# Performance work log

Measured on AMD Instinct MI355X. Metric: run time of the kernel, lower is better.

Reference implementation:

```python
import jax, jax.numpy as jnp
import numpy as np

N_NODES = 50000
NEG_SLOPE = 0.01  # F.leaky_relu default


def setup_inputs() -> dict:
    key = jax.random.key(0)
    k1, k2, k3, k4, k5 = jax.random.split(key, 5)
    in_dim, out_dim, n_edges = 256, 64, 800000
    h = jax.random.normal(k1, (N_NODES, in_dim), dtype=jnp.float32)
    edge_src = jax.random.randint(k2, (n_edges,), 0, N_NODES, dtype=jnp.int32)
    edge_dst = jax.random.randint(k3, (n_edges,), 0, N_NODES, dtype=jnp.int32)
    W_fc = jax.random.normal(k4, (in_dim, out_dim), dtype=jnp.float32) / np.sqrt(in_dim)
    a_attn = jax.random.normal(k5, (2 * out_dim,), dtype=jnp.float32) / np.sqrt(2 * out_dim)
    return {"h": h, "edge_src": edge_src, "edge_dst": edge_dst, "W_fc": W_fc, "a_attn": a_attn}


def reference(h, edge_src, edge_dst, W_fc, a_attn):
    # z = fc(h)
    z = h @ W_fc                                   # [N, D]
    D = z.shape[1]
    # cat([z_src, z_dst]) @ a == z_src @ a_l + z_dst @ a_r (no edge concat materialized)
    a_l, a_r = a_attn[:D], a_attn[D:]
    s_l = z @ a_l                                  # [N]
    s_r = z @ a_r                                  # [N]
    e = s_l[edge_src] + s_r[edge_dst]              # [E]
    e = jnp.where(e > 0, e, NEG_SLOPE * e)         # leaky_relu
    # segment softmax over incoming edges of each dst node (DGL mailbox softmax)
    m = jax.ops.segment_max(e, edge_dst, num_segments=N_NODES)   # -inf for isolated nodes
    ex = jnp.exp(e - m[edge_dst])                  # [E]
    den = jax.ops.segment_sum(ex, edge_dst, num_segments=N_NODES)
    alpha = ex / den[edge_dst]                     # [E]
    # weighted neighbor aggregation: h_v = sum_{u->v} alpha * z_u
    msgs = alpha[:, None] * z[edge_src]            # [E, D]
    h_out = jax.ops.segment_sum(msgs, edge_dst, num_segments=N_NODES)  # [N, D]
    return h_out
```

## Files before the change

### kernel.cpp

```cpp
#include <hip/hip_runtime.h>

#define IN_DIM   256
#define OUT_DIM  64
#define NEG_SLOPE 0.01f
#define KPAD (IN_DIM + 8)
#define MAXBUCK 2048
#define CAP     1024
#define EPB     4096

typedef __attribute__((ext_vector_type(8))) short short8;
typedef __attribute__((ext_vector_type(4))) float f32x4;
typedef unsigned short ushort_t;

__device__ inline unsigned f2bf_u(float f) {
    unsigned u = __float_as_uint(f);
    return (u + 0x7FFF + ((u >> 16) & 1)) >> 16;
}
__device__ inline short f2bf(float f) { return (short)f2bf_u(f); }
__device__ inline float bf2f(unsigned u16) { return __uint_as_float(u16 << 16); }

__global__ __launch_bounds__(256)
void prep_kernel(const float* __restrict__ W, short* __restrict__ Wt,
                 int* __restrict__ cnt, int nbuck)
{
    const int g = blockIdx.x * 256 + threadIdx.x;
    for (int i = g; i < nbuck; i += 8 * 256) cnt[i] = 0;
    for (int i = g; i < IN_DIM * OUT_DIM; i += 8 * 256) {
        const int k = i & (IN_DIM - 1);
        const int n = i >> 8;
        Wt[i] = f2bf(W[(size_t)k * OUT_DIM + n]);
    }
}

__global__ __launch_bounds__(256, 4)
void fused_kernel(const float* __restrict__ h, const short* __restrict__ Wt,
                  const float* __restrict__ a_attn,
                  ushort_t* __restrict__ z_bf, float* __restrict__ s_l,
                  float* __restrict__ s_r,
                  const int* __restrict__ esrc, const int* __restrict__ edst,
                  int* __restrict__ cnt, unsigned* __restrict__ perm,
                  int n_nodes, int n_edges, int nbuck, int ms_blocks)
{
    __shared__ union {
        short As[64 * KPAD];
        struct { int hist[MAXBUCK]; int cur[MAXBUCK]; } m;
    } sm;

    const int tid = threadIdx.x;

    if ((int)blockIdx.x < ms_blocks) {
        for (int i = tid; i < nbuck; i += 256) sm.m.hist[i] = 0;
        __syncthreads();
        const int base = blockIdx.x * EPB;
        unsigned pw[EPB / 256];
#pragma unroll
        for (int j = 0; j < EPB / 256; ++j) {
            const int i = base + j * 256 + tid;
            unsigned w = 0xFFFFFFFFu;
            if (i < n_edges) {
                const int d = edst[i];
                w = ((unsigned)d << 16) | (unsigned)esrc[i];
                atomicAdd(&sm.m.hist[d >> 5], 1);
            }
            pw[j] = w;
        }
        __syncthreads();
        for (int i = tid; i < nbuck; i += 256) {
            const int hv = sm.m.hist[i];
            if (hv) sm.m.cur[i] = i * CAP + atomicAdd(&cnt[i], hv);
        }
        __syncthreads();
#pragma unroll
        for (int j = 0; j < EPB / 256; ++j) {
            const unsigned w = pw[j];
            if (w != 0xFFFFFFFFu) {
                const int bk = (int)(w >> 21);
                const int pos = atomicAdd(&sm.m.cur[bk], 1);
                if (pos < (bk + 1) * CAP) perm[pos] = w;
            }
        }
        return;
    }

    const int wave = tid >> 6;
    const int lane = tid & 63;
    const int nbase = ((int)blockIdx.x - ms_blocks) * 64;

    for (int i = tid; i < 64 * (IN_DIM / 4); i += 256) {
        const int m  = i >> 6;
        const int k4 = i & 63;
        int node = nbase + m;
        if (node >= n_nodes) node = n_nodes - 1;
        const float4 h4 = *(const float4*)&h[(size_t)node * IN_DIM + k4 * 4];
        uint2 p;
        p.x = f2bf_u(h4.x) | (f2bf_u(h4.y) << 16);
        p.y = f2bf_u(h4.z) | (f2bf_u(h4.w) << 16);
        *(uint2*)&sm.As[m * KPAD + k4 * 4] = p;
    }
    __syncthreads();

    f32x4 acc[4];
#pragma unroll
    for (int t = 0; t < 4; ++t) acc[t] = (f32x4){0.f, 0.f, 0.f, 0.f};

    const int col0 = lane & 15;
    const int quad = lane >> 4;
    const int mrow = wave * 16 + col0;
    const int kq   = quad * 8;

#pragma unroll
    for (int ks = 0; ks < IN_DIM / 32; ++ks) {
        const int kb = ks * 32 + kq;
        const short8 a = *(const short8*)&sm.As[mrow * KPAD + kb];
#pragma unroll
        for (int t = 0; t < 4; ++t) {
            const short8 b = *(const short8*)&Wt[(t * 16 + col0) * IN_DIM + kb];
            acc[t] = __builtin_amdgcn_mfma_f32_16x16x32_bf16(a, b, acc[t], 0, 0, 0);
        }
    }

    float al[4], ar[4];
#pragma unroll
    for (int t = 0; t < 4; ++t) {
        al[t] = a_attn[t * 16 + col0];
        ar[t] = a_attn[OUT_DIM + t * 16 + col0];
    }
#pragma unroll
    for (int r = 0; r < 4; ++r) {
        const int m = nbase + wave * 16 + quad * 4 + r;
        const bool live = m < n_nodes;
        float sl = 0.f, sr = 0.f;
#pragma unroll
        for (int t = 0; t < 4; ++t) {
            const float v = acc[t][r];
            if (live) z_bf[(size_t)m * OUT_DIM + t * 16 + col0] = (ushort_t)f2bf(v);
            sl += v * al[t];
            sr += v * ar[t];
        }
#pragma unroll
        for (int off = 1; off < 16; off <<= 1) {
            sl += __shfl_xor(sl, off, 16);
            sr += __shfl_xor(sr, off, 16);
        }
        if (live && col0 == 0) { s_l[m] = sl; s_r[m] = sr; }
    }
}

__global__ __launch_bounds__(512)
void gather_kernel(const unsigned* __restrict__ perm, const int* __restrict__ cnt,
                   const float* __restrict__ s_l, const float* __restrict__ s_r,
                   const ushort_t* __restrict__ z_bf, float* __restrict__ out,
                   int n_nodes)
{
    __shared__ unsigned eds[CAP];
    __shared__ ushort_t srcs[CAP];
    __shared__ int hist[32], starts[33], cur[32];

    const int tid = threadIdx.x;
    const int b   = blockIdx.x;
    int nE = cnt[b];
    if (nE > CAP) nE = CAP;

    if (tid < 32) hist[tid] = 0;
    __syncthreads();

    for (int i = tid; i < nE; i += 512) {
        const unsigned p = perm[(size_t)b * CAP + i];
        eds[i] = p;
        atomicAdd(&hist[(p >> 16) & 31], 1);
    }
    __syncthreads();

    if (tid < 32) {
        const int v = hist[tid];
        int inc = v;
#pragma unroll
        for (int off = 1; off < 32; off <<= 1) {
            const int u = __shfl_up(inc, off, 32);
            if (tid >= off) inc += u;
        }
        starts[tid + 1] = inc;
        cur[tid] = inc - v;
        if (tid == 0) starts[0] = 0;
    }
    __syncthreads();

    for (int i = tid; i < nE; i += 512) {
        const unsigned p = eds[i];
        const int pos = atomicAdd(&cur[(p >> 16) & 31], 1);
        srcs[pos] = (ushort_t)(p & 0xFFFFu);
    }
    __syncthreads();

    const int ld = tid >> 4;
    const int c  = tid & 15;
    const int d  = b * 32 + ld;
    if (d >= n_nodes) return;

    int k = starts[ld];
    const int ke = starts[ld + 1];
    const float srd = s_r[d];

    float a0 = 0.f, a1 = 0.f, a2 = 0.f, a3 = 0.f, den = 0.f;

    for (; k + 8 <= ke; k += 8) {
        int   s[8];
        float l[8];
        uint2 q[8];
#pragma unroll
        for (int j = 0; j < 8; ++j) s[j] = srcs[k + j];
#pragma unroll
        for (int j = 0; j < 8; ++j) {
            l[j] = s_l[s[j]];
            q[j] = *(const uint2*)&z_bf[(size_t)s[j] * OUT_DIM + c * 4];
        }
#pragma unroll
        for (int j = 0; j < 8; ++j) {
            float e = l[j] + srd;
            e = e > 0.f ? e : NEG_SLOPE * e;
            const float x = __expf(e);
            den += x;
            a0 += x * bf2f(q[j].x & 0xFFFFu);
            a1 += x * bf2f(q[j].x >> 16);
            a2 += x * bf2f(q[j].y & 0xFFFFu);
            a3 += x * bf2f(q[j].y >> 16);
        }
    }
    for (; k + 4 <= ke; k += 4) {
        int   s[4];
        float l[4];
        uint2 q[4];
#pragma unroll
        for (int j = 0; j < 4; ++j) s[j] = srcs[k + j];
#pragma unroll
        for (int j = 0; j < 4; ++j) {
            l[j] = s_l[s[j]];
            q[j] = *(const uint2*)&z_bf[(size_t)s[j] * OUT_DIM + c * 4];
        }
#pragma unroll
        for (int j = 0; j < 4; ++j) {
            float e = l[j] + srd;
            e = e > 0.f ? e : NEG_SLOPE * e;
            const float x = __expf(e);
            den += x;
            a0 += x * bf2f(q[j].x & 0xFFFFu);
            a1 += x * bf2f(q[j].x >> 16);
            a2 += x * bf2f(q[j].y & 0xFFFFu);
            a3 += x * bf2f(q[j].y >> 16);
        }
    }
    for (; k < ke; ++k) {
        const int s0 = srcs[k];
        float e = s_l[s0] + srd;
        e = e > 0.f ? e : NEG_SLOPE * e;
        const float x = __expf(e);
        const uint2 q0 = *(const uint2*)&z_bf[(size_t)s0 * OUT_DIM + c * 4];
        den += x;
        a0 += x * bf2f(q0.x & 0xFFFFu);
        a1 += x * bf2f(q0.x >> 16);
        a2 += x * bf2f(q0.y & 0xFFFFu);
        a3 += x * bf2f(q0.y >> 16);
    }

    const float inv = den > 0.f ? 1.f / den : 0.f;
    float4 o;
    o.x = a0 * inv; o.y = a1 * inv; o.z = a2 * inv; o.w = a3 * inv;
    *(float4*)&out[(size_t)d * OUT_DIM + c * 4] = o;
}

extern "C" void kernel_launch(void* const* d_in, const int* in_sizes, int n_in,
                              void* d_out, int out_size, void* d_ws, size_t ws_size,
                              hipStream_t stream)
{
    const float* h        = (const float*)d_in[0];
    const int*   edge_src = (const int*)  d_in[1];
    const int*   edge_dst = (const int*)  d_in[2];
    const float* W        = (const float*)d_in[3];
    const float* a_attn   = (const float*)d_in[4];
    float*       out      = (float*)d_out;

    const int n_nodes = in_sizes[0] / IN_DIM;
    const int n_edges = in_sizes[1];
    const int nbuck   = (n_nodes + 31) >> 5;

    char* wsb = (char*)d_ws;
    short*    Wt   = (short*)wsb;
    size_t off = (size_t)IN_DIM * OUT_DIM * sizeof(short);
    ushort_t* z_bf = (ushort_t*)(wsb + off);
    off += (size_t)n_nodes * OUT_DIM * sizeof(ushort_t);
    float*    s_l  = (float*)(wsb + off);  off += (size_t)n_nodes * 4;
    float*    s_r  = (float*)(wsb + off);  off += (size_t)n_nodes * 4;
    int*      cnt  = (int*)(wsb + off);    off += ((size_t)nbuck * 4 + 15) & ~(size_t)15;
    unsigned* perm = (unsigned*)(wsb + off);

    const int ms_blocks   = (n_edges + EPB - 1) / EPB;
    const int gemm_blocks = (n_nodes + 63) / 64;

    prep_kernel<<<8, 256, 0, stream>>>(W, Wt, cnt, nbuck);
    fused_kernel<<<ms_blocks + gemm_blocks, 256, 0, stream>>>(
        h, Wt, a_attn, z_bf, s_l, s_r, edge_src, edge_dst, cnt, perm,
        n_nodes, n_edges, nbuck, ms_blocks);
    gather_kernel<<<nbuck, 512, 0, stream>>>(
        perm, cnt, s_l, s_r, z_bf, out, n_nodes);
}
```

Before: 133.9 us.

## Split each node's edge list across two 8-lane groups with 16-byte loads

The gather kernel now has each destination node's incoming edges handled by two groups of 8 lanes, each covering half the edge range. Each lane loads 8 bf16 features with one 16-byte load instead of 4 with an 8-byte load. The two partial sums and denominators are combined through shared memory after a block barrier and then normalized and written out. This is meant to shorten per-node dependency chains and widen memory transactions. It costs extra shared memory and a sync, and removes the 4-edge unrolled remainder loop.

```diff
diff --git a/kernel.cpp b/kernel.cpp
--- a/kernel.cpp
+++ b/kernel.cpp
@@ -154,6 +154,8 @@
 {
     __shared__ unsigned eds[CAP];
     __shared__ ushort_t srcs[CAP];
+    __shared__ float accH[2][32][OUT_DIM];
+    __shared__ float denH[2][32];
     __shared__ int hist[32], starts[33], cur[32];
 
     const int tid = threadIdx.x;
@@ -192,27 +194,34 @@
     }
     __syncthreads();
 
-    const int ld = tid >> 4;
-    const int c  = tid & 15;
-    const int d  = b * 32 + ld;
-    if (d >= n_nodes) return;
-
-    int k = starts[ld];
-    const int ke = starts[ld + 1];
-    const float srd = s_r[d];
-
-    float a0 = 0.f, a1 = 0.f, a2 = 0.f, a3 = 0.f, den = 0.f;
+    const int grp  = tid >> 3;
+    const int ld   = grp >> 1;
+    const int half = grp & 1;
+    const int c2   = tid & 7;
+    const int d    = b * 32 + ld;
+
+    const int begin = starts[ld];
+    const int end   = starts[ld + 1];
+    const int mid   = begin + ((end - begin + 1) >> 1);
+    int k  = half ? mid : begin;
+    const int ke = half ? end : mid;
+    const float srd = (d < n_nodes) ? s_r[d] : 0.f;
+
+    float a[8];
+#pragma unroll
+    for (int t = 0; t < 8; ++t) a[t] = 0.f;
+    float den = 0.f;
 
     for (; k + 8 <= ke; k += 8) {
         int   s[8];
         float l[8];
-        uint2 q[8];
+        uint4 q[8];
 #pragma unroll
         for (int j = 0; j < 8; ++j) s[j] = srcs[k + j];
 #pragma unroll
         for (int j = 0; j < 8; ++j) {
             l[j] = s_l[s[j]];
-            q[j] = *(const uint2*)&z_bf[(size_t)s[j] * OUT_DIM + c * 4];
+            q[j] = *(const uint4*)&z_bf[(size_t)s[j] * OUT_DIM + c2 * 8];
         }
 #pragma unroll
         for (int j = 0; j < 8; ++j) {
@@ -220,33 +229,14 @@
             e = e > 0.f ? e : NEG_SLOPE * e;
             const float x = __expf(e);
             den += x;
-            a0 += x * bf2f(q[j].x & 0xFFFFu);
-            a1 += x * bf2f(q[j].x >> 16);
-            a2 += x * bf2f(q[j].y & 0xFFFFu);
-            a3 += x * bf2f(q[j].y >> 16);
-        }
-    }
-    for (; k + 4 <= ke; k += 4) {
-        int   s[4];
-        float l[4];
-        uint2 q[4];
-#pragma unroll
-        for (int j = 0; j < 4; ++j) s[j] = srcs[k + j];
-#pragma unroll
-        for (int j = 0; j < 4; ++j) {
-            l[j] = s_l[s[j]];
-            q[j] = *(const uint2*)&z_bf[(size_t)s[j] * OUT_DIM + c * 4];
-        }
-#pragma unroll
-        for (int j = 0; j < 4; ++j) {
-            float e = l[j] + srd;
-            e = e > 0.f ? e : NEG_SLOPE * e;
-            const float x = __expf(e);
-            den += x;
-            a0 += x * bf2f(q[j].x & 0xFFFFu);
-            a1 += x * bf2f(q[j].x >> 16);
-            a2 += x * bf2f(q[j].y & 0xFFFFu);
-            a3 += x * bf2f(q[j].y >> 16);
+            a[0] += x * bf2f(q[j].x & 0xFFFFu);
+            a[1] += x * bf2f(q[j].x >> 16);
+            a[2] += x * bf2f(q[j].y & 0xFFFFu);
+            a[3] += x * bf2f(q[j].y >> 16);
+            a[4] += x * bf2f(q[j].z & 0xFFFFu);
+            a[5] += x * bf2f(q[j].z >> 16);
+            a[6] += x * bf2f(q[j].w & 0xFFFFu);
+            a[7] += x * bf2f(q[j].w >> 16);
         }
     }
     for (; k < ke; ++k) {
@@ -254,18 +244,40 @@
         float e = s_l[s0] + srd;
         e = e > 0.f ? e : NEG_SLOPE * e;
         const float x = __expf(e);
-        const uint2 q0 = *(const uint2*)&z_bf[(size_t)s0 * OUT_DIM + c * 4];
+        const uint4 q0 = *(const uint4*)&z_bf[(size_t)s0 * OUT_DIM + c2 * 8];
         den += x;
-        a0 += x * bf2f(q0.x & 0xFFFFu);
-        a1 += x * bf2f(q0.x >> 16);
-        a2 += x * bf2f(q0.y & 0xFFFFu);
-        a3 += x * bf2f(q0.y >> 16);
-    }
-
-    const float inv = den > 0.f ? 1.f / den : 0.f;
-    float4 o;
-    o.x = a0 * inv; o.y = a1 * inv; o.z = a2 * inv; o.w = a3 * inv;
-    *(float4*)&out[(size_t)d * OUT_DIM + c * 4] = o;
+        a[0] += x * bf2f(q0.x & 0xFFFFu);
+        a[1] += x * bf2f(q0.x >> 16);
+        a[2] += x * bf2f(q0.y & 0xFFFFu);
+        a[3] += x * bf2f(q0.y >> 16);
+        a[4] += x * bf2f(q0.z & 0xFFFFu);
+        a[5] += x * bf2f(q0.z >> 16);
+        a[6] += x * bf2f(q0.w & 0xFFFFu);
+        a[7] += x * bf2f(q0.w >> 16);
+    }
+
+#pragma unroll
+    for (int t = 0; t < 8; ++t) accH[half][ld][c2 * 8 + t] = a[t];
+    if (c2 == 0) denH[half][ld] = den;
+    __syncthreads();
+
+    for (int i = tid; i < 32 * 16; i += 512) {
+        const int l2 = i >> 4;
+        const int cq = i & 15;
+        const int dd = b * 32 + l2;
+        if (dd < n_nodes) {
+            const float dn = denH[0][l2] + denH[1][l2];
+            const float inv = dn > 0.f ? 1.f / dn : 0.f;
+            const float* r0 = &accH[0][l2][cq * 4];
+            const float* r1 = &accH[1][l2][cq * 4];
+            float4 o;
+            o.x = (r0[0] + r1[0]) * inv;
+            o.y = (r0[1] + r1[1]) * inv;
+            o.z = (r0[2] + r1[2]) * inv;
+            o.w = (r0[3] + r1[3]) * inv;
+            *(float4*)&out[(size_t)dd * OUT_DIM + cq * 4] = o;
+        }
+    }
 }
 
 extern "C" void kernel_launch(void* const* d_in, const int* in_sizes, int n_in,
```

New measurement: 138.2 us. 1.03x slower.
